# Optimization experiments

Measured on AMD Instinct MI355X. Metric: run time of the kernel, lower is better.

## Reference

```python
import jax, jax.numpy as jnp
import numpy as np

K = 16          # buckets per codeblock (2**treeDepth)
DEPTH = 4       # tree depth
C = 256         # codeblockCount
IN_FEATURES = 4096
OUT_FEATURES = 4096
N_ROWS = 4096

_BASE_TREE = np.array([
    [-1,-1,0,-1,0,0,0,-1,0,0,0,0,0,0,0],[-1,-1,0,-1,0,0,0,1,0,0,0,0,0,0,0],
    [-1,-1,0,1,0,0,0,0,-1,0,0,0,0,0,0],[-1,-1,0,1,0,0,0,0,1,0,0,0,0,0,0],
    [-1,1,0,0,-1,0,0,0,0,-1,0,0,0,0,0],[-1,1,0,0,-1,0,0,0,0,1,0,0,0,0,0],
    [-1,1,0,0,1,0,0,0,0,0,-1,0,0,0,0],[-1,1,0,0,1,0,0,0,0,0,1,0,0,0,0],
    [1,0,-1,0,0,-1,0,0,0,0,0,-1,0,0,0],[1,0,-1,0,0,-1,0,0,0,0,0,1,0,0,0],
    [1,0,-1,0,0,1,0,0,0,0,0,0,-1,0,0],[1,0,-1,0,0,1,0,0,0,0,0,0,1,0,0],
    [1,0,1,0,0,0,-1,0,0,0,0,0,0,-1,0],[1,0,1,0,0,0,-1,0,0,0,0,0,0,1,0],
    [1,0,1,0,0,0,1,0,0,0,0,0,0,0,-1],[1,0,1,0,0,0,1,0,0,0,0,0,0,0,1]],
    dtype=np.float32)

def _make_tree_des_matrix(c):
    # NOTE: original code initializes with ONES, then overwrites diagonal blocks
    m = np.ones((c * K, c * (K - 1)), dtype=np.float32)
    for i in range(c):
        m[i*K:(i+1)*K, i*(K-1):(i+1)*(K-1)] = _BASE_TREE
    return m

def _make_selection_matrix(c):
    base = np.zeros((K - 1, DEPTH), dtype=np.float32)
    base[0, 0] = 1.0
    for i in range(1, K - 1):
        base[i, int(np.log2(i + 1))] = 1.0
    m = np.zeros((c * (K - 1), c * DEPTH), dtype=np.float32)
    for i in range(c):
        m[i*(K-1):(i+1)*(K-1), i*DEPTH:(i+1)*DEPTH] = base
    return m

def setup_inputs() -> dict:
    key = jax.random.key(0)
    k1, k2, k3, k4 = jax.random.split(key, 4)
    inputMatrix = jax.random.normal(k1, (N_ROWS, IN_FEATURES), dtype=jnp.float32)
    dims = jax.random.randint(k2, (C * DEPTH,), 0, IN_FEATURES)
    selection_matrix = jnp.asarray(_make_selection_matrix(C))
    thresholds = jax.random.normal(k3, (C * (K - 1), 1), dtype=jnp.float32)
    tree_des_mat = jnp.asarray(_make_tree_des_matrix(C))
    lut = jax.random.normal(k4, (OUT_FEATURES, C, K), dtype=jnp.float32)
    return {"inputMatrix": inputMatrix, "dims": dims,
            "selection_matrix": selection_matrix, "thresholds": thresholds,
            "tree_des_mat": tree_des_mat, "lut": lut}

def reference(inputMatrix, dims, selection_matrix, thresholds, tree_des_mat, lut):
    n = inputMatrix.shape[0]
    c = lut.shape[1]
    # gather the tree-split feature dims: (N, C*DEPTH)
    chosen = inputMatrix[:, dims]
    # (C*15, N)
    subtracted = selection_matrix @ chosen.T - thresholds
    tanh_h = jnp.tanh(subtracted)
    sign_ste = jnp.sign(subtracted) - jax.lax.stop_gradient(tanh_h) + tanh_h
    # (C*16, N) -> (N, C, 16)
    tree_result = (tree_des_mat @ sign_ste).T.reshape(n, c, K)
    encoding_soft = jax.nn.softmax(tree_result, axis=2)
    index = jnp.argmax(encoding_soft, axis=2)
    encoding_hard = jax.nn.one_hot(index, K, dtype=encoding_soft.dtype)
    Encoded = encoding_hard - jax.lax.stop_gradient(encoding_soft) + encoding_soft
    # LUT lookup: einsum 'nij,kij->nki' + sum over i, fused to 'nij,kij->nk'
    out = jnp.einsum('nij,kij->nk', Encoded, lut)
    return out
```

## Files before the change

kernel.cpp:

```cpp
#include <hip/hip_runtime.h>

#define N_ROWS 4096
#define IN_F   4096
#define OUT_F  4096
#define C_CB   256
#define KDIM   4096

typedef short bf16x8 __attribute__((ext_vector_type(8)));
typedef float f32x4  __attribute__((ext_vector_type(4)));

union ABFrag { unsigned long long u[2]; bf16x8 v; };

__device__ __forceinline__ unsigned int f2bf(float f) {
    unsigned int u = __builtin_bit_cast(unsigned int, f);
    return (u + 0x7FFFu + ((u >> 16) & 1u)) >> 16;
}

__global__ void k_idx(const float* __restrict__ input, const int* __restrict__ dims,
                      const float* __restrict__ thr, unsigned char* __restrict__ idx8) {
    const int n = blockIdx.x;
    const int c = threadIdx.x;
    const float* row = input + (size_t)n * IN_F;
    int4 d = *(const int4*)(dims + c * 4);
    const float* th = thr + c * 15;
    float x0 = row[d.x], x1 = row[d.y], x2 = row[d.z], x3 = row[d.w];
    int b0 = x0 > th[0];
    int j1 = 1 + b0;
    int b1 = x1 > th[j1];
    int j2 = 2 * j1 + 1 + b1;
    int b2 = x2 > th[j2];
    int j3 = 2 * j2 + 1 + b2;
    int b3 = x3 > th[j3];
    idx8[n * C_CB + c] = (unsigned char)((b0 << 3) | (b1 << 2) | (b2 << 1) | b3);
}

__global__ void k_cvt(const float* __restrict__ lut, unsigned short* __restrict__ lutb) {
    const int i = (blockIdx.x * blockDim.x + threadIdx.x) * 8;
    float4 a = *(const float4*)(lut + i);
    float4 b = *(const float4*)(lut + i + 4);
    uint4 o;
    o.x = f2bf(a.x) | (f2bf(a.y) << 16);
    o.y = f2bf(a.z) | (f2bf(a.w) << 16);
    o.z = f2bf(b.x) | (f2bf(b.y) << 16);
    o.w = f2bf(b.z) | (f2bf(b.w) << 16);
    *(uint4*)(lutb + i) = o;
}

#define BM 128
#define BN 128
#define BKT 64
#define IDXP 272

template<bool STAGE_FP32>
__global__ __launch_bounds__(256, 2) void k_gemm(const unsigned short* __restrict__ lutb,
                                                 const float* __restrict__ lutf,
                                                 const unsigned char* __restrict__ idx8,
                                                 float* __restrict__ out) {
    __shared__ unsigned char smem[128 * IDXP + BN * BKT * 2];
    unsigned char* ish = smem;
    unsigned char* bsh = smem + 128 * IDXP;

    const int t   = threadIdx.x;
    const int l15 = t & 15;
    const int q   = (t >> 4) & 3;
    const int w   = t >> 6;
    const int wm  = w >> 1, wn = w & 1;
    const int m0  = blockIdx.y * BM;
    const int n0  = blockIdx.x * BN;

    {
        int r = t >> 1, h = t & 1;
        const uint4* src = (const uint4*)(idx8 + (size_t)(m0 + r) * C_CB + h * 128);
        uint4* dst = (uint4*)(ish + r * IDXP + h * 128);
        #pragma unroll
        for (int i = 0; i < 8; i++) dst[i] = src[i];
    }

    f32x4 acc[4][4];
    #pragma unroll
    for (int mi = 0; mi < 4; mi++)
        #pragma unroll
        for (int ni = 0; ni < 4; ni++)
            acc[mi][ni] = (f32x4){0.f, 0.f, 0.f, 0.f};

    const int xorv = l15 & 7;
    const int bRowByte = (wn * 64 + l15) * (BKT * 2);
    const int aRowBase = (wm * 64 + l15) * IDXP;

    for (int kb = 0; kb < KDIM; kb += BKT) {
        if (!STAGE_FP32) {
            #pragma unroll
            for (int qq = 0; qq < 4; qq++) {
                int L = qq * 256 + t;
                int r = L >> 3, p = L & 7;
                int c = p ^ (r & 7);
                const unsigned short* g = lutb + (size_t)(n0 + r) * KDIM + kb + c * 8;
                __builtin_amdgcn_global_load_lds(
                    (const __attribute__((address_space(1))) void*)g,
                    (__attribute__((address_space(3))) void*)(bsh + L * 16), 16, 0, 0);
            }
        } else {
            #pragma unroll
            for (int qq = 0; qq < 4; qq++) {
                int L = qq * 256 + t;
                int r = L >> 3, p = L & 7;
                int c = p ^ (r & 7);
                const float* g = lutf + (size_t)(n0 + r) * KDIM + kb + c * 8;
                float4 f0 = *(const float4*)g;
                float4 f1 = *(const float4*)(g + 4);
                uint4 o;
                o.x = f2bf(f0.x) | (f2bf(f0.y) << 16);
                o.y = f2bf(f0.z) | (f2bf(f0.w) << 16);
                o.z = f2bf(f1.x) | (f2bf(f1.y) << 16);
                o.w = f2bf(f1.z) | (f2bf(f1.w) << 16);
                *(uint4*)(bsh + L * 16) = o;
            }
        }
        __syncthreads();

        #pragma unroll
        for (int s = 0; s < 2; s++) {
            const int c0 = (kb >> 4) + 2 * s;

            ABFrag bf[4];
            const int chunkOff = ((s * 4 + q) ^ xorv) * 16;
            #pragma unroll
            for (int ni = 0; ni < 4; ni++)
                bf[ni].v = *(const bf16x8*)(bsh + bRowByte + ni * (16 * BKT * 2) + chunkOff);

            ABFrag af[4];
            #pragma unroll
            for (int mi = 0; mi < 4; mi++) {
                unsigned int v = *(const unsigned short*)(ish + aRowBase + mi * 16 * IDXP + c0);
                unsigned int idx0 = v & 0xFFu, idx1 = v >> 8;
                unsigned int T = (q >> 1) ? idx1 : idx0;
                unsigned int rel = T - ((q & 1) << 3);
                unsigned long long sh = 0x3F80ull << ((rel & 3) << 4);
                af[mi].u[0] = (rel < 4u) ? sh : 0ull;
                af[mi].u[1] = ((rel - 4u) < 4u) ? sh : 0ull;
            }

            #pragma unroll
            for (int mi = 0; mi < 4; mi++)
                #pragma unroll
                for (int ni = 0; ni < 4; ni++)
                    acc[mi][ni] = __builtin_amdgcn_mfma_f32_16x16x32_bf16(
                        af[mi].v, bf[ni].v, acc[mi][ni], 0, 0, 0);
        }
        __syncthreads();
    }

    #pragma unroll
    for (int mi = 0; mi < 4; mi++) {
        #pragma unroll
        for (int ni = 0; ni < 4; ni++) {
            const int row0 = m0 + wm * 64 + mi * 16 + q * 4;
            const int col  = n0 + wn * 64 + ni * 16 + l15;
            #pragma unroll
            for (int r = 0; r < 4; r++)
                out[(size_t)(row0 + r) * OUT_F + col] = acc[mi][ni][r];
        }
    }
}

extern "C" void kernel_launch(void* const* d_in, const int* in_sizes, int n_in,
                              void* d_out, int out_size, void* d_ws, size_t ws_size,
                              hipStream_t stream) {
    const float* input = (const float*)d_in[0];
    const int*   dims  = (const int*)d_in[1];
    const float* thr   = (const float*)d_in[3];
    const float* lut   = (const float*)d_in[5];
    float* out = (float*)d_out;

    const size_t lutbBytes = (size_t)OUT_F * KDIM * 2;
    const size_t idxBytes  = (size_t)N_ROWS * C_CB;

    dim3 gg(OUT_F / BN, N_ROWS / BM);

    if (ws_size >= lutbBytes + idxBytes) {
        unsigned short* lutb = (unsigned short*)d_ws;
        unsigned char*  idx8 = (unsigned char*)d_ws + lutbBytes;
        k_idx<<<N_ROWS, C_CB, 0, stream>>>(input, dims, thr, idx8);
        k_cvt<<<(OUT_F * KDIM) / (256 * 8), 256, 0, stream>>>(lut, lutb);
        k_gemm<false><<<gg, 256, 0, stream>>>(lutb, lut, idx8, out);
    } else {
        unsigned char* idx8 = (unsigned char*)d_ws;
        k_idx<<<N_ROWS, C_CB, 0, stream>>>(input, dims, thr, idx8);
        k_gemm<true><<<gg, 256, 0, stream>>>(nullptr, lut, idx8, out);
    }
}
```

Before: 325.7 us.

## Pack bucket indices as nibbles in codeblock-major layout and shrink GEMM LDS

The index kernel now packs two 4-bit bucket indices per byte and stores them transposed, codeblock-pair major by row. The GEMM loads this smaller index tile into LDS with async global_load_lds, which cuts LDS from about 50KB to 32KB. Launch bounds are raised to 4 blocks per SM to allow more occupancy. The A-fragment rows are permuted so one 32-bit LDS read serves all four mi tiles, and the output row mapping is adjusted to match.

```diff
diff --git a/kernel.cpp b/kernel.cpp
--- a/kernel.cpp
+++ b/kernel.cpp
@@ -17,7 +17,7 @@
 }
 
 __global__ void k_idx(const float* __restrict__ input, const int* __restrict__ dims,
-                      const float* __restrict__ thr, unsigned char* __restrict__ idx8) {
+                      const float* __restrict__ thr, unsigned char* __restrict__ idx4) {
     const int n = blockIdx.x;
     const int c = threadIdx.x;
     const float* row = input + (size_t)n * IN_F;
@@ -31,7 +31,10 @@
     int b2 = x2 > th[j2];
     int j3 = 2 * j2 + 1 + b2;
     int b3 = x3 > th[j3];
-    idx8[n * C_CB + c] = (unsigned char)((b0 << 3) | (b1 << 2) | (b2 << 1) | b3);
+    int idx = (b0 << 3) | (b1 << 2) | (b2 << 1) | b3;
+    int other = __shfl_xor(idx, 1);
+    if (!(c & 1))
+        idx4[(c >> 1) * N_ROWS + n] = (unsigned char)(idx | (other << 4));
 }
 
 __global__ void k_cvt(const float* __restrict__ lut, unsigned short* __restrict__ lutb) {
@@ -49,16 +52,15 @@
 #define BM 128
 #define BN 128
 #define BKT 64
-#define IDXP 272
 
 template<bool STAGE_FP32>
-__global__ __launch_bounds__(256, 2) void k_gemm(const unsigned short* __restrict__ lutb,
+__global__ __launch_bounds__(256, 4) void k_gemm(const unsigned short* __restrict__ lutb,
                                                  const float* __restrict__ lutf,
-                                                 const unsigned char* __restrict__ idx8,
+                                                 const unsigned char* __restrict__ idx4,
                                                  float* __restrict__ out) {
-    __shared__ unsigned char smem[128 * IDXP + BN * BKT * 2];
+    __shared__ unsigned char smem[16384 + BN * BKT * 2];
     unsigned char* ish = smem;
-    unsigned char* bsh = smem + 128 * IDXP;
+    unsigned char* bsh = smem + 16384;
 
     const int t   = threadIdx.x;
     const int l15 = t & 15;
@@ -68,12 +70,13 @@
     const int m0  = blockIdx.y * BM;
     const int n0  = blockIdx.x * BN;
 
-    {
-        int r = t >> 1, h = t & 1;
-        const uint4* src = (const uint4*)(idx8 + (size_t)(m0 + r) * C_CB + h * 128);
-        uint4* dst = (uint4*)(ish + r * IDXP + h * 128);
-        #pragma unroll
-        for (int i = 0; i < 8; i++) dst[i] = src[i];
+    #pragma unroll
+    for (int qq = 0; qq < 4; qq++) {
+        int L = qq * 256 + t;
+        const unsigned char* g = idx4 + (size_t)(L >> 3) * N_ROWS + m0 + (L & 7) * 16;
+        __builtin_amdgcn_global_load_lds(
+            (const __attribute__((address_space(1))) void*)g,
+            (__attribute__((address_space(3))) void*)(ish + L * 16), 16, 0, 0);
     }
 
     f32x4 acc[4][4];
@@ -85,7 +88,9 @@
 
     const int xorv = l15 & 7;
     const int bRowByte = (wn * 64 + l15) * (BKT * 2);
-    const int aRowBase = (wm * 64 + l15) * IDXP;
+    const int aByte = wm * 64 + l15 * 4;
+    const int qh4  = (q >> 1) * 4;
+    const unsigned int sub8 = (q & 1) << 3;
 
     for (int kb = 0; kb < KDIM; kb += BKT) {
         if (!STAGE_FP32) {
@@ -120,7 +125,7 @@
 
         #pragma unroll
         for (int s = 0; s < 2; s++) {
-            const int c0 = (kb >> 4) + 2 * s;
+            const int cbp = (kb >> 5) + s;
 
             ABFrag bf[4];
             const int chunkOff = ((s * 4 + q) ^ xorv) * 16;
@@ -128,13 +133,13 @@
             for (int ni = 0; ni < 4; ni++)
                 bf[ni].v = *(const bf16x8*)(bsh + bRowByte + ni * (16 * BKT * 2) + chunkOff);
 
+            const unsigned int w32 = *(const unsigned int*)(ish + cbp * 128 + aByte);
+
             ABFrag af[4];
             #pragma unroll
             for (int mi = 0; mi < 4; mi++) {
-                unsigned int v = *(const unsigned short*)(ish + aRowBase + mi * 16 * IDXP + c0);
-                unsigned int idx0 = v & 0xFFu, idx1 = v >> 8;
-                unsigned int T = (q >> 1) ? idx1 : idx0;
-                unsigned int rel = T - ((q & 1) << 3);
+                unsigned int T = (w32 >> (mi * 8 + qh4)) & 0xFu;
+                unsigned int rel = T - sub8;
                 unsigned long long sh = 0x3F80ull << ((rel & 3) << 4);
                 af[mi].u[0] = (rel < 4u) ? sh : 0ull;
                 af[mi].u[1] = ((rel - 4u) < 4u) ? sh : 0ull;
@@ -154,11 +159,12 @@
     for (int mi = 0; mi < 4; mi++) {
         #pragma unroll
         for (int ni = 0; ni < 4; ni++) {
-            const int row0 = m0 + wm * 64 + mi * 16 + q * 4;
-            const int col  = n0 + wn * 64 + ni * 16 + l15;
+            const int col = n0 + wn * 64 + ni * 16 + l15;
             #pragma unroll
-            for (int r = 0; r < 4; r++)
-                out[(size_t)(row0 + r) * OUT_F + col] = acc[mi][ni][r];
+            for (int r = 0; r < 4; r++) {
+                const int row = m0 + wm * 64 + 4 * (q * 4 + r) + mi;
+                out[(size_t)row * OUT_F + col] = acc[mi][ni][r];
+            }
         }
     }
 }
@@ -173,19 +179,19 @@
     float* out = (float*)d_out;
 
     const size_t lutbBytes = (size_t)OUT_F * KDIM * 2;
-    const size_t idxBytes  = (size_t)N_ROWS * C_CB;
+    const size_t idxBytes  = (size_t)(C_CB / 2) * N_ROWS;
 
     dim3 gg(OUT_F / BN, N_ROWS / BM);
 
     if (ws_size >= lutbBytes + idxBytes) {
         unsigned short* lutb = (unsigned short*)d_ws;
-        unsigned char*  idx8 = (unsigned char*)d_ws + lutbBytes;
-        k_idx<<<N_ROWS, C_CB, 0, stream>>>(input, dims, thr, idx8);
+        unsigned char*  idx4 = (unsigned char*)d_ws + lutbBytes;
+        k_idx<<<N_ROWS, C_CB, 0, stream>>>(input, dims, thr, idx4);
         k_cvt<<<(OUT_F * KDIM) / (256 * 8), 256, 0, stream>>>(lut, lutb);
-        k_gemm<false><<<gg, 256, 0, stream>>>(lutb, lut, idx8, out);
+        k_gemm<false><<<gg, 256, 0, stream>>>(lutb, lut, idx4, out);
     } else {
-        unsigned char* idx8 = (unsigned char*)d_ws;
-        k_idx<<<N_ROWS, C_CB, 0, stream>>>(input, dims, thr, idx8);
-        k_gemm<true><<<gg, 256, 0, stream>>>(nullptr, lut, idx8, out);
+        unsigned char* idx4 = (unsigned char*)d_ws;
+        k_idx<<<N_ROWS, C_CB, 0, stream>>>(input, dims, thr, idx4);
+        k_gemm<true><<<gg, 256, 0, stream>>>(nullptr, lut, idx4, out);
     }
 }
```

After: 314.5 us. 1.04x faster.
